# Kernel optimization log

Hardware: AMD Instinct MI355X
Metric: run time of the kernel (lower is better)

## Reference

```python
import jax, jax.numpy as jnp
from jax import lax
import numpy as np

B, IMG, P, CIN, D, DEPTH, H, FF = 32, 512, 16, 4, 256, 4, 8, 2048
N = (IMG // P) ** 2          # 1024 patches
L = N // 2                   # exactly 512 masked patches per batch (static max_len)
DH = D // H
EPS = 1e-5


def layer_norm(x, s, b):
    m = x.mean(-1, keepdims=True)
    v = ((x - m) ** 2).mean(-1, keepdims=True)
    return (x - m) * lax.rsqrt(v + EPS) * s + b


def setup_inputs() -> dict:
    key = jax.random.key(0)
    ks = jax.random.split(key, 16)
    init = lambda k, shp: 0.02 * jax.random.normal(k, shp, jnp.float32)

    image = jax.random.normal(ks[0], (B, 3, IMG, IMG), jnp.float32)
    # patch-granular binary mask: exactly L patches per batch have value 0 (masked)
    scores = jax.random.uniform(ks[1], (B, N))
    idx = jnp.argsort(scores, axis=1)[:, :L]
    pm = jnp.ones((B, N), jnp.float32).at[jnp.arange(B)[:, None], idx].set(0.0)
    mask = jnp.repeat(jnp.repeat(pm.reshape(B, 1, IMG // P, IMG // P), P, 2), P, 3)

    return dict(
        image=image, mask=mask,
        conv_w=init(ks[2], (D, CIN, P, P)), conv_b=jnp.zeros((D,), jnp.float32),
        pos_embed=jax.random.normal(ks[3], (1, N, D), jnp.float32),
        qkv_w=init(ks[4], (DEPTH, D, 3 * D)), qkv_b=jnp.zeros((DEPTH, 3 * D), jnp.float32),
        out_w=init(ks[5], (DEPTH, D, D)), out_b=jnp.zeros((DEPTH, D), jnp.float32),
        ln1_s=jnp.ones((DEPTH, D), jnp.float32), ln1_b=jnp.zeros((DEPTH, D), jnp.float32),
        ff1_w=init(ks[6], (DEPTH, D, FF)), ff1_b=jnp.zeros((DEPTH, FF), jnp.float32),
        ff2_w=init(ks[7], (DEPTH, FF, D)), ff2_b=jnp.zeros((DEPTH, D), jnp.float32),
        ln2_s=jnp.ones((DEPTH, D), jnp.float32), ln2_b=jnp.zeros((DEPTH, D), jnp.float32),
    )


def reference(image, mask, conv_w, conv_b, pos_embed, qkv_w, qkv_b, out_w, out_b,
              ln1_s, ln1_b, ff1_w, ff1_b, ff2_w, ff2_b, ln2_s, ln2_b):
    xin = jnp.concatenate([image, mask], axis=1)                       # [B,4,512,512]
    x = lax.conv_general_dilated(xin, conv_w, (P, P), 'VALID',
                                 dimension_numbers=('NCHW', 'OIHW', 'NCHW'))
    x = x + conv_b[None, :, None, None]                                # [B,D,32,32]
    Bc = x.shape[0]
    x = x.reshape(Bc, D, N).transpose(0, 2, 1)                         # [B,N,D]

    # nearest downsample (factor exactly P): sample at indices i*P
    pmask = mask[:, 0, ::P, ::P].reshape(Bc, N)
    sel = pmask < 0.5                                                  # masked patches
    # stable compaction: indices of masked patches first, in original order
    order = jnp.argsort(jnp.logical_not(sel), axis=1, stable=True)[:, :L]
    tokens = jnp.take_along_axis(x, order[..., None], axis=1)          # [B,L,D]
    pos = pos_embed[0][order]                                          # [B,L,D]
    lengths = sel.sum(axis=1)
    valid = (jnp.arange(L)[None, :] < lengths[:, None])[..., None]
    h = jnp.where(valid, tokens + pos, 0.0)                            # zero padding

    scale = 1.0 / np.sqrt(DH)
    for i in range(DEPTH):  # post-norm torch TransformerEncoderLayer, no dropout
        qkv = h @ qkv_w[i] + qkv_b[i]
        q, k, v = jnp.split(qkv, 3, axis=-1)
        q = q.reshape(Bc, L, H, DH)
        k = k.reshape(Bc, L, H, DH)
        v = v.reshape(Bc, L, H, DH)
        att = jax.nn.softmax(jnp.einsum('bqhd,bkhd->bhqk', q, k) * scale, axis=-1)
        o = jnp.einsum('bhqk,bkhd->bqhd', att, v).reshape(Bc, L, D)
        h = layer_norm(h + o @ out_w[i] + out_b[i], ln1_s[i], ln1_b[i])
        ff = jax.nn.relu(h @ ff1_w[i] + ff1_b[i]) @ ff2_w[i] + ff2_b[i]
        h = layer_norm(h + ff, ln2_s[i], ln2_b[i])
    return h
```

## Files before the change

kernel.cpp:

```cpp
#include <hip/hip_runtime.h>
#include <cstdint>
#include <cstddef>


#define Bq 32
#define Dm 256
#define Lq 512
#define Hh 8
#define FFq 2048
#define Mtok (Bq * Lq)

typedef __attribute__((ext_vector_type(8))) short  short8;
typedef __attribute__((ext_vector_type(4))) float  f32x4;
typedef __attribute__((ext_vector_type(4))) unsigned int u32x4;
typedef __attribute__((ext_vector_type(2))) unsigned int u32x2;

static __device__ __forceinline__ unsigned short f2bf(float f) {
    unsigned int u = __float_as_uint(f);
    unsigned int r = (u + 0x7FFFu + ((u >> 16) & 1u)) >> 16;
    return (unsigned short)r;
}
static __device__ __forceinline__ unsigned int pk2bf(float lo, float hi) {
    return (unsigned int)f2bf(lo) | ((unsigned int)f2bf(hi) << 16);
}

static __device__ __forceinline__ void gload_lds16(const void* g, void* l) {
    __builtin_amdgcn_global_load_lds(
        (const __attribute__((address_space(1))) unsigned int*)g,
        (__attribute__((address_space(3))) unsigned int*)l, 16, 0, 0);
}

static __device__ __forceinline__ int xcd_swz(int id, int grid) {
    return (id & 7) * (grid >> 3) + (id >> 3);
}

__global__ __launch_bounds__(1024) void k_order(const float* __restrict__ mask,
                                                int* __restrict__ order) {
    const int b = blockIdx.x;
    const int n = threadIdx.x;
    const float v = mask[(size_t)b * 262144 + (size_t)(n >> 5) * 8192 + (n & 31) * 16];
    const bool sel = v < 0.5f;
    const unsigned long long ball = __ballot(sel);
    const int wave = n >> 6, lane = n & 63;
    __shared__ int wsum[16];
    __shared__ int wpre[16];
    if (lane == 0) wsum[wave] = __popcll(ball);
    __syncthreads();
    if (n == 0) {
        int s = 0;
        for (int i = 0; i < 16; ++i) { wpre[i] = s; s += wsum[i]; }
    }
    __syncthreads();
    const int rank = wpre[wave] + __popcll(ball & ((1ull << lane) - 1ull));
    if (sel) order[b * Lq + rank] = n;
}

__global__ __launch_bounds__(256) void k_gather(const float* __restrict__ image,
                                                const int* __restrict__ order,
                                                const float* __restrict__ pos,
                                                unsigned short* __restrict__ patchA,
                                                float* __restrict__ posG) {
    __shared__ int pn[16];
    const int tid = threadIdx.x;
    const int tok0 = blockIdx.x * 16;
    if (tid < 16) pn[tid] = order[tok0 + tid];
    __syncthreads();
    const int lane = tid & 63, w4 = tid >> 6;
    const int rr = lane >> 2, col4 = (lane & 3) << 2;
#pragma unroll
    for (int it = 0; it < 12; ++it) {
        const int s = it * 4 + w4;
        const int t = s / 3, cch = s % 3;
        const int n = pn[t];
        const int b = (tok0 + t) >> 9;
        const int pi = n >> 5, pj = n & 31;
        const float4 v = *(const float4*)&image[
            (((size_t)b * 3 + cch) * 512 + pi * 16 + rr) * 512 + pj * 16 + col4];
        unsigned int pk[2] = {pk2bf(v.x, v.y), pk2bf(v.z, v.w)};
        *(uint2*)&patchA[(size_t)(tok0 + t) * 768 + cch * 256 + rr * 16 + col4] =
            *(uint2*)pk;
    }
#pragma unroll
    for (int it = 0; it < 4; ++it) {
        const int t = it * 4 + w4;
        *(float4*)&posG[(size_t)(tok0 + t) * Dm + lane * 4] =
            *(const float4*)&pos[(size_t)pn[t] * Dm + lane * 4];
    }
}

__global__ __launch_bounds__(256) void k_wembed(const float* __restrict__ conv_w,
                                                unsigned short* __restrict__ W16) {
    const int i = blockIdx.x * 256 + threadIdx.x;
    const int d = i / 96, k8 = (i % 96) * 8;
    const float4 a = *(const float4*)&conv_w[(size_t)d * 1024 + k8];
    const float4 b = *(const float4*)&conv_w[(size_t)d * 1024 + k8 + 4];
    unsigned int pk[4] = {pk2bf(a.x, a.y), pk2bf(a.z, a.w),
                          pk2bf(b.x, b.y), pk2bf(b.z, b.w)};
    *(uint4*)&W16[(size_t)d * 768 + k8] = *(uint4*)pk;
}

__global__ __launch_bounds__(256) void k_wprep_all(const float* __restrict__ qkv_w,
                                                   const float* __restrict__ out_w,
                                                   const float* __restrict__ ff1_w,
                                                   const float* __restrict__ ff2_w,
                                                   unsigned short* __restrict__ Wq,
                                                   unsigned short* __restrict__ Wo,
                                                   unsigned short* __restrict__ Wf1,
                                                   unsigned short* __restrict__ Wf2) {
    __shared__ float tile[64][65];
    int idx = blockIdx.x;
    const float* W; unsigned short* WT; int K, N, l, r;
    if (idx < 192)      { l = idx / 48;          r = idx % 48;  K = 256;  N = 768;  W = qkv_w; WT = Wq; }
    else if (idx < 256) { l = (idx - 192) / 16;  r = idx & 15;  K = 256;  N = 256;  W = out_w; WT = Wo; }
    else if (idx < 768) { l = (idx - 256) / 128; r = (idx - 256) % 128; K = 256;  N = 2048; W = ff1_w; WT = Wf1; }
    else                { l = (idx - 768) / 128; r = (idx - 768) % 128; K = 2048; N = 256;  W = ff2_w; WT = Wf2; }
    const int nTiles = N >> 6;
    const int n0 = (r % nTiles) * 64, k0 = (r / nTiles) * 64;
    W  += (size_t)l * K * N;
    WT += (size_t)l * K * N;
    const int t = threadIdx.x;
#pragma unroll
    for (int it = 0; it < 4; ++it) {
        const int rr = (t >> 4) + it * 16, c4 = (t & 15) * 4;
        *(float4*)&tile[rr][c4] = *(const float4*)&W[(size_t)(k0 + rr) * N + n0 + c4];
    }
    __syncthreads();
    const int n = t & 63, kq = t >> 6;
    unsigned short pk[16];
#pragma unroll
    for (int j = 0; j < 16; ++j) pk[j] = f2bf(tile[kq * 16 + j][n]);
    unsigned short* dst = &WT[(size_t)(n0 + n) * K + k0 + kq * 16];
    *(uint4*)dst       = *(uint4*)&pk[0];
    *(uint4*)(dst + 8) = *(uint4*)&pk[8];
}

template <bool RELU, bool RES, bool OUT32, bool OUT16, int NBUF, bool SWZ>
__global__ __launch_bounds__(256) void k_mgemm(const unsigned short* __restrict__ A,
                                               const unsigned short* __restrict__ W,
                                               const float* __restrict__ bias,
                                               const float* __restrict__ R,
                                               float* __restrict__ C32,
                                               unsigned short* __restrict__ C16,
                                               int ntiles, int M, int N, int K) {
    __shared__ unsigned short Al[128 * 64 * NBUF];
    __shared__ unsigned short Bl[128 * 64 * NBUF];
    const int tid = threadIdx.x;
    const int lane = tid & 63, wave = tid >> 6;
    const int wm = wave >> 1, wn = wave & 1;
    int id = blockIdx.x;
    if constexpr (SWZ) id = xcd_swz(id, (int)gridDim.x);
    const int n0 = (id % ntiles) * 128, m0 = (id / ntiles) * 128;
    const int c = lane >> 4, a15 = lane & 15;
    f32x4 acc[4][4] = {};

    const int srow = lane >> 3;
    const int sgran = (lane & 7) ^ srow;
    const int KT = K >> 6;

    auto stage = [&](int buf, int kt) {
        const int k0 = kt << 6;
#pragma unroll
        for (int q = 0; q < 4; ++q) {
            const int rbase = wave * 32 + q * 8;
            gload_lds16(A + (size_t)(m0 + rbase + srow) * K + k0 + sgran * 8,
                        &Al[buf * 8192 + rbase * 64]);
            gload_lds16(W + (size_t)(n0 + rbase + srow) * K + k0 + sgran * 8,
                        &Bl[buf * 8192 + rbase * 64]);
        }
    };
    auto compute = [&](int buf) {
        const int bo = buf * 8192;
#pragma unroll
        for (int kc = 0; kc < 2; ++kc) {
            short8 af[4], bf[4];
#pragma unroll
            for (int fm = 0; fm < 4; ++fm) {
                const int row = wm * 64 + fm * 16 + a15;
                const int slot = (kc * 4 + c) ^ (row & 7);
                af[fm] = *(const short8*)&Al[bo + row * 64 + slot * 8];
            }
#pragma unroll
            for (int fn = 0; fn < 4; ++fn) {
                const int row = wn * 64 + fn * 16 + a15;
                const int slot = (kc * 4 + c) ^ (row & 7);
                bf[fn] = *(const short8*)&Bl[bo + row * 64 + slot * 8];
            }
#pragma unroll
            for (int fm = 0; fm < 4; ++fm)
#pragma unroll
                for (int fn = 0; fn < 4; ++fn)
                    acc[fm][fn] = __builtin_amdgcn_mfma_f32_16x16x32_bf16(
                        af[fm], bf[fn], acc[fm][fn], 0, 0, 0);
        }
    };

    if constexpr (NBUF == 2) {
        stage(0, 0);
        for (int kt = 0; kt < KT; ++kt) {
            const int cur = kt & 1;
            if (kt + 1 < KT) {
                stage(cur ^ 1, kt + 1);
                asm volatile("s_waitcnt vmcnt(8)" ::: "memory");
            } else {
                asm volatile("s_waitcnt vmcnt(0)" ::: "memory");
            }
            __builtin_amdgcn_s_barrier();
            compute(cur);
            __builtin_amdgcn_s_barrier();
        }
    } else {
        for (int kt = 0; kt < KT; ++kt) {
            __syncthreads();
            stage(0, kt);
            __syncthreads();
            compute(0);
        }
    }
#pragma unroll
    for (int fn = 0; fn < 4; ++fn) {
        const int col = n0 + wn * 64 + fn * 16 + a15;
        const float bv = bias[col];
#pragma unroll
        for (int fm = 0; fm < 4; ++fm) {
            const int mrow = m0 + wm * 64 + fm * 16 + c * 4;
#pragma unroll
            for (int r = 0; r < 4; ++r) {
                float v = acc[fm][fn][r] + bv;
                if constexpr (RES) v += R[(size_t)(mrow + r) * N + col];
                if constexpr (RELU) v = fmaxf(v, 0.f);
                if constexpr (OUT32) C32[(size_t)(mrow + r) * N + col] = v;
                if constexpr (OUT16) C16[(size_t)(mrow + r) * N + col] = f2bf(v);
            }
        }
    }
}

template <bool RELU, bool OUT16>
__global__ __launch_bounds__(512) void k_mgemm8(const unsigned short* __restrict__ A,
                                                const unsigned short* __restrict__ W,
                                                const float* __restrict__ bias,
                                                unsigned short* __restrict__ C16,
                                                int ntiles, int N, int K) {
    __shared__ unsigned short Al[256 * 64];
    __shared__ unsigned short Bl[128 * 64];
    const int tid = threadIdx.x;
    const int lane = tid & 63, wave = tid >> 6;
    const int wm = wave >> 1, wn = wave & 1;
    const int id = xcd_swz((int)blockIdx.x, (int)gridDim.x);
    const int n0 = (id % ntiles) * 128, m0 = (id / ntiles) * 256;
    const int c = lane >> 4, a15 = lane & 15;
    f32x4 acc[4][4] = {};

    const int srow = lane >> 3;
    const int sgran = (lane & 7) ^ srow;
    const int KT = K >> 6;

    for (int kt = 0; kt < KT; ++kt) {
        const int k0 = kt << 6;
        __syncthreads();
#pragma unroll
        for (int q = 0; q < 4; ++q) {
            const int rbase = wave * 32 + q * 8;
            gload_lds16(A + (size_t)(m0 + rbase + srow) * K + k0 + sgran * 8,
                        &Al[rbase * 64]);
        }
#pragma unroll
        for (int q = 0; q < 2; ++q) {
            const int rbase = wave * 16 + q * 8;
            gload_lds16(W + (size_t)(n0 + rbase + srow) * K + k0 + sgran * 8,
                        &Bl[rbase * 64]);
        }
        __syncthreads();
#pragma unroll
        for (int kc = 0; kc < 2; ++kc) {
            short8 af[4], bf[4];
#pragma unroll
            for (int fm = 0; fm < 4; ++fm) {
                const int row = wm * 64 + fm * 16 + a15;
                const int slot = (kc * 4 + c) ^ (row & 7);
                af[fm] = *(const short8*)&Al[row * 64 + slot * 8];
            }
#pragma unroll
            for (int fn = 0; fn < 4; ++fn) {
                const int row = wn * 64 + fn * 16 + a15;
                const int slot = (kc * 4 + c) ^ (row & 7);
                bf[fn] = *(const short8*)&Bl[row * 64 + slot * 8];
            }
#pragma unroll
            for (int fm = 0; fm < 4; ++fm)
#pragma unroll
                for (int fn = 0; fn < 4; ++fn)
                    acc[fm][fn] = __builtin_amdgcn_mfma_f32_16x16x32_bf16(
                        af[fm], bf[fn], acc[fm][fn], 0, 0, 0);
        }
    }
#pragma unroll
    for (int fn = 0; fn < 4; ++fn) {
        const int col = n0 + wn * 64 + fn * 16 + a15;
        const float bv = bias[col];
#pragma unroll
        for (int fm = 0; fm < 4; ++fm) {
            const int mrow = m0 + wm * 64 + fm * 16 + c * 4;
#pragma unroll
            for (int r = 0; r < 4; ++r) {
                float v = acc[fm][fn][r] + bv;
                if constexpr (RELU) v = fmaxf(v, 0.f);
                if constexpr (OUT16) C16[(size_t)(mrow + r) * N + col] = f2bf(v);
            }
        }
    }
}

__global__ __launch_bounds__(256) void k_gemm_ln(const unsigned short* __restrict__ A,
                                                 const unsigned short* __restrict__ W,
                                                 const float* __restrict__ bias,
                                                 const float* __restrict__ R,
                                                 const float* __restrict__ lns,
                                                 const float* __restrict__ lnb,
                                                 float* __restrict__ Y32,
                                                 unsigned short* __restrict__ Y16,
                                                 int K) {
    __shared__ unsigned short Al[32 * 64 * 2];
    __shared__ unsigned short Bl[256 * 64 * 2];
    __shared__ float redS[4][32];
    __shared__ float redQ[4][32];
    const int tid = threadIdx.x;
    const int lane = tid & 63, wave = tid >> 6;
    const int m0 = xcd_swz((int)blockIdx.x, (int)gridDim.x) * 32;
    const int c = lane >> 4, a15 = lane & 15;
    f32x4 acc[2][4] = {};

    const int srow = lane >> 3;
    const int sgran = (lane & 7) ^ srow;
    const int KT = K >> 6;

    auto stage = [&](int buf, int kt) {
        const int k0 = kt << 6;
        gload_lds16(A + (size_t)(m0 + wave * 8 + srow) * K + k0 + sgran * 8,
                    &Al[buf * 2048 + (wave * 8) * 64]);
#pragma unroll
        for (int q = 0; q < 8; ++q) {
            const int rbase = wave * 64 + q * 8;
            gload_lds16(W + (size_t)(rbase + srow) * K + k0 + sgran * 8,
                        &Bl[buf * 16384 + rbase * 64]);
        }
    };
    auto compute = [&](int buf) {
        const int ao = buf * 2048, bo = buf * 16384;
#pragma unroll
        for (int kc = 0; kc < 2; ++kc) {
            short8 af[2], bf[4];
#pragma unroll
            for (int fm = 0; fm < 2; ++fm) {
                const int row = fm * 16 + a15;
                const int slot = (kc * 4 + c) ^ (row & 7);
                af[fm] = *(const short8*)&Al[ao + row * 64 + slot * 8];
            }
#pragma unroll
            for (int fn = 0; fn < 4; ++fn) {
                const int row = wave * 64 + fn * 16 + a15;
                const int slot = (kc * 4 + c) ^ (row & 7);
                bf[fn] = *(const short8*)&Bl[bo + row * 64 + slot * 8];
            }
#pragma unroll
            for (int fm = 0; fm < 2; ++fm)
#pragma unroll
                for (int fn = 0; fn < 4; ++fn)
                    acc[fm][fn] = __builtin_amdgcn_mfma_f32_16x16x32_bf16(
                        af[fm], bf[fn], acc[fm][fn], 0, 0, 0);
        }
    };

    stage(0, 0);
    for (int kt = 0; kt < KT; ++kt) {
        const int cur = kt & 1;
        if (kt + 1 < KT) {
            stage(cur ^ 1, kt + 1);
            asm volatile("s_waitcnt vmcnt(9)" ::: "memory");
        } else {
            asm volatile("s_waitcnt vmcnt(0)" ::: "memory");
        }
        __builtin_amdgcn_s_barrier();
        compute(cur);
        __builtin_amdgcn_s_barrier();
    }

    float bv[4], sg[4], bg[4];
#pragma unroll
    for (int fn = 0; fn < 4; ++fn) {
        const int col = wave * 64 + fn * 16 + a15;
        bv[fn] = bias[col]; sg[fn] = lns[col]; bg[fn] = lnb[col];
    }
#pragma unroll
    for (int fm = 0; fm < 2; ++fm) {
        const int mrow = m0 + fm * 16 + c * 4;
#pragma unroll
        for (int r = 0; r < 4; ++r) {
            float ps = 0.f, pq = 0.f;
#pragma unroll
            for (int fn = 0; fn < 4; ++fn) {
                const int col = wave * 64 + fn * 16 + a15;
                float v = acc[fm][fn][r] + bv[fn] + R[(size_t)(mrow + r) * Dm + col];
                acc[fm][fn][r] = v;
                ps += v; pq += v * v;
            }
#pragma unroll
            for (int off = 1; off < 16; off <<= 1) {
                ps += __shfl_xor(ps, off);
                pq += __shfl_xor(pq, off);
            }
            if (a15 == 0) {
                redS[wave][fm * 16 + c * 4 + r] = ps;
                redQ[wave][fm * 16 + c * 4 + r] = pq;
            }
        }
    }
    __syncthreads();
#pragma unroll
    for (int fm = 0; fm < 2; ++fm) {
        const int lrow = fm * 16 + c * 4;
        const int mrow = m0 + lrow;
#pragma unroll
        for (int r = 0; r < 4; ++r) {
            const float totS = redS[0][lrow + r] + redS[1][lrow + r] +
                               redS[2][lrow + r] + redS[3][lrow + r];
            const float totQ = redQ[0][lrow + r] + redQ[1][lrow + r] +
                               redQ[2][lrow + r] + redQ[3][lrow + r];
            const float mean = totS * (1.f / 256.f);
            const float var = totQ * (1.f / 256.f) - mean * mean;
            const float inv = rsqrtf(var + 1e-5f);
#pragma unroll
            for (int fn = 0; fn < 4; ++fn) {
                const int col = wave * 64 + fn * 16 + a15;
                const float y = (acc[fm][fn][r] - mean) * inv * sg[fn] + bg[fn];
                Y32[(size_t)(mrow + r) * Dm + col] = y;
                Y16[(size_t)(mrow + r) * Dm + col] = f2bf(y);
            }
        }
    }
}

__global__ __launch_bounds__(512) void k_attn(const unsigned short* __restrict__ QKV,
                                              unsigned short* __restrict__ O) {
    __shared__ unsigned short Kl[512 * 32];
    __shared__ unsigned short Vt[32 * 512];
    const int bh = xcd_swz((int)blockIdx.x, (int)gridDim.x);
    const int b = bh >> 3, h = bh & 7;
    const int tid = threadIdx.x, lane = tid & 63, wave = tid >> 6;
    const int c = lane >> 4, a15 = lane & 15;
    const size_t qkvbase = (size_t)b * Lq * 768 + h * 32;

    {
        const int srow = lane >> 2;
        const int sg = (lane & 3) ^ ((srow >> 1) & 3);
#pragma unroll
        for (int q = 0; q < 4; ++q) {
            const int rbase = wave * 64 + q * 16;
            gload_lds16(QKV + qkvbase + (size_t)(rbase + srow) * 768 + 256 + sg * 8,
                        &Kl[rbase * 32]);
        }
    }
    {
        const int kg = tid & 127, dg = tid >> 7;
        u32x4 v[4];
#pragma unroll
        for (int kk = 0; kk < 4; ++kk)
            v[kk] = *(const u32x4*)&QKV[qkvbase + (size_t)(kg * 4 + kk) * 768 + 512 + dg * 8];
#pragma unroll
        for (int dd = 0; dd < 8; ++dd) {
            const int d = dg * 8 + dd;
            unsigned short e[4];
#pragma unroll
            for (int kk = 0; kk < 4; ++kk) {
                const unsigned int word = v[kk][dd >> 1];
                e[kk] = (dd & 1) ? (unsigned short)(word >> 16) : (unsigned short)(word & 0xffff);
            }
            unsigned int pk[2];
            pk[0] = (unsigned int)e[0] | ((unsigned int)e[1] << 16);
            pk[1] = (unsigned int)e[2] | ((unsigned int)e[3] << 16);
            *(uint2*)&Vt[d * 512 + ((kg ^ (d & 7)) << 2)] = *(uint2*)pk;
        }
    }
    const int q0w = wave * 64;
    short8 qf[4];
#pragma unroll
    for (int fn = 0; fn < 4; ++fn)
        qf[fn] = *(const short8*)&QKV[qkvbase + (size_t)(q0w + fn * 16 + a15) * 768 + c * 8];
    __syncthreads();

    const float scale = 0.17677669529663687f;
    f32x4 oacc[2][4] = {};
    float mstat[4], lstat[4];
#pragma unroll
    for (int fn = 0; fn < 4; ++fn) { mstat[fn] = -1e30f; lstat[fn] = 0.f; }
    const f32x4 zero4 = {0.f, 0.f, 0.f, 0.f};

    for (int t = 0; t < 16; ++t) {
        const int kv0 = t * 32;
        short8 kf[2];
#pragma unroll
        for (int fm = 0; fm < 2; ++fm) {
            const int row = kv0 + fm * 16 + a15;
            const int slot = c ^ ((row >> 1) & 3);
            kf[fm] = *(const short8*)&Kl[row * 32 + slot * 8];
        }
        short8 vf[2];
#pragma unroll
        for (int fmd = 0; fmd < 2; ++fmd) {
            const int d = fmd * 16 + a15;
            const int g0 = (t * 8 + c) ^ (d & 7);
            const int g1 = (t * 8 + 4 + c) ^ (d & 7);
            const u32x2 r0 = *(const u32x2*)&Vt[d * 512 + g0 * 4];
            const u32x2 r1 = *(const u32x2*)&Vt[d * 512 + g1 * 4];
            const u32x4 cmb = {r0[0], r0[1], r1[0], r1[1]};
            vf[fmd] = __builtin_bit_cast(short8, cmb);
        }
        f32x4 s[2][4];
#pragma unroll
        for (int fm = 0; fm < 2; ++fm)
#pragma unroll
            for (int fn = 0; fn < 4; ++fn)
                s[fm][fn] = __builtin_amdgcn_mfma_f32_16x16x32_bf16(kf[fm], qf[fn], zero4, 0, 0, 0);
#pragma unroll
        for (int fn = 0; fn < 4; ++fn) {
            float p[8];
            float tmax = -1e30f;
#pragma unroll
            for (int fm = 0; fm < 2; ++fm)
#pragma unroll
                for (int r = 0; r < 4; ++r) {
                    const float x = s[fm][fn][r] * scale;
                    p[fm * 4 + r] = x;
                    tmax = fmaxf(tmax, x);
                }
            tmax = fmaxf(tmax, __shfl_xor(tmax, 16));
            tmax = fmaxf(tmax, __shfl_xor(tmax, 32));
            const float mnew = fmaxf(mstat[fn], tmax);
            const float alpha = __expf(mstat[fn] - mnew);
            mstat[fn] = mnew;
            float tsum = 0.f;
            short8 pf;
#pragma unroll
            for (int j = 0; j < 8; ++j) {
                const float e = __expf(p[j] - mnew);
                tsum += e;
                pf[j] = (short)f2bf(e);
            }
            tsum += __shfl_xor(tsum, 16);
            tsum += __shfl_xor(tsum, 32);
            lstat[fn] = lstat[fn] * alpha + tsum;
#pragma unroll
            for (int fmd = 0; fmd < 2; ++fmd) {
                oacc[fmd][fn] *= alpha;
                oacc[fmd][fn] = __builtin_amdgcn_mfma_f32_16x16x32_bf16(
                    vf[fmd], pf, oacc[fmd][fn], 0, 0, 0);
            }
        }
    }
#pragma unroll
    for (int fn = 0; fn < 4; ++fn) {
        const float invl = 1.f / lstat[fn];
        const size_t qrow = (size_t)(b * Lq + q0w + fn * 16 + a15);
#pragma unroll
        for (int fmd = 0; fmd < 2; ++fmd)
#pragma unroll
            for (int r = 0; r < 4; ++r)
                O[qrow * Dm + h * 32 + fmd * 16 + c * 4 + r] = f2bf(oacc[fmd][fn][r] * invl);
    }
}

extern "C" void kernel_launch(void* const* d_in, const int* in_sizes, int n_in,
                              void* d_out, int out_size, void* d_ws, size_t ws_size,
                              hipStream_t stream) {
    const float* image  = (const float*)d_in[0];
    const float* mask   = (const float*)d_in[1];
    const float* conv_w = (const float*)d_in[2];
    const float* conv_b = (const float*)d_in[3];
    const float* pos    = (const float*)d_in[4];
    const float* qkv_w  = (const float*)d_in[5];
    const float* qkv_b  = (const float*)d_in[6];
    const float* out_w  = (const float*)d_in[7];
    const float* out_b  = (const float*)d_in[8];
    const float* ln1_s  = (const float*)d_in[9];
    const float* ln1_b  = (const float*)d_in[10];
    const float* ff1_w  = (const float*)d_in[11];
    const float* ff1_b  = (const float*)d_in[12];
    const float* ff2_w  = (const float*)d_in[13];
    const float* ff2_b  = (const float*)d_in[14];
    const float* ln2_s  = (const float*)d_in[15];
    const float* ln2_b  = (const float*)d_in[16];
    float* out = (float*)d_out;

    char* w = (char*)d_ws;
    int* order            = (int*)w;            w += 64 * 1024;
    float* H32            = (float*)w;          w += (size_t)Mtok * Dm * 4;
    unsigned short* H16   = (unsigned short*)w; w += (size_t)Mtok * Dm * 2;
    unsigned short* QKV16 = (unsigned short*)w; w += (size_t)Mtok * 768 * 2;
    unsigned short* O16   = (unsigned short*)w; w += (size_t)Mtok * Dm * 2;
    unsigned short* F16   = (unsigned short*)w; w += (size_t)Mtok * FFq * 2;
    unsigned short* Wq    = (unsigned short*)w; w += (size_t)4 * 768 * 256 * 2;
    unsigned short* Wo    = (unsigned short*)w; w += (size_t)4 * 256 * 256 * 2;
    unsigned short* Wf1   = (unsigned short*)w; w += (size_t)4 * 2048 * 256 * 2;
    unsigned short* Wf2   = (unsigned short*)w; w += (size_t)4 * 256 * 2048 * 2;
    unsigned short* We    = (unsigned short*)w; w += (size_t)256 * 768 * 2;
    unsigned short* patchA = F16;
    float* posG            = (float*)(F16 + (size_t)Mtok * 768);

    k_order<<<Bq, 1024, 0, stream>>>(mask, order);
    k_gather<<<Mtok / 16, 256, 0, stream>>>(image, order, pos, patchA, posG);
    k_wembed<<<96, 256, 0, stream>>>(conv_w, We);
    k_wprep_all<<<1280, 256, 0, stream>>>(qkv_w, out_w, ff1_w, ff2_w, Wq, Wo, Wf1, Wf2);

    k_mgemm<false, true, true, true, 2, true><<<256, 256, 0, stream>>>(
        patchA, We, conv_b, posG, H32, H16, 2, Mtok, 256, 768);

    for (int i = 0; i < 4; ++i) {
        k_mgemm8<false, true><<<384, 512, 0, stream>>>(
            H16, Wq + (size_t)i * 768 * 256, qkv_b + (size_t)i * 768,
            QKV16, 6, 768, 256);
        k_attn<<<Bq * Hh, 512, 0, stream>>>(QKV16, O16);
        k_gemm_ln<<<Mtok / 32, 256, 0, stream>>>(
            O16, Wo + (size_t)i * 256 * 256, out_b + (size_t)i * 256, H32,
            ln1_s + i * Dm, ln1_b + i * Dm, H32, H16, 256);
        k_mgemm8<true, true><<<1024, 512, 0, stream>>>(
            H16, Wf1 + (size_t)i * 2048 * 256, ff1_b + (size_t)i * FFq,
            F16, 16, 2048, 256);
        float* dst32 = (i == 3) ? out : H32;
        k_gemm_ln<<<Mtok / 32, 256, 0, stream>>>(
            F16, Wf2 + (size_t)i * 256 * 2048, ff2_b + (size_t)i * 256, H32,
            ln2_s + i * Dm, ln2_b + i * Dm, dst32, H16, 2048);
    }
    (void)in_sizes; (void)n_in; (void)out_size; (void)ws_size;
}
```

Measured before the change: 552.6 us.

## Widen fused GEMM+LayerNorm tile to 64 rows with 8 waves

The fused GEMM+residual+LayerNorm kernel now processes 64 rows per block with 512 threads in a 2x4 wave grid, instead of 32 rows with 4 waves. Each staged weight tile is shared by twice as many rows, which halves total weight traffic from global memory into LDS. The grid shrinks from 512 to 256 blocks, roughly one per CU, and LDS use per block rises. This may reduce occupancy and latency hiding.

```diff
diff --git a/kernel.cpp b/kernel.cpp
--- a/kernel.cpp
+++ b/kernel.cpp
@@ -311,22 +311,23 @@
     }
 }
 
-__global__ __launch_bounds__(256) void k_gemm_ln(const unsigned short* __restrict__ A,
-                                                 const unsigned short* __restrict__ W,
-                                                 const float* __restrict__ bias,
-                                                 const float* __restrict__ R,
-                                                 const float* __restrict__ lns,
-                                                 const float* __restrict__ lnb,
-                                                 float* __restrict__ Y32,
-                                                 unsigned short* __restrict__ Y16,
-                                                 int K) {
-    __shared__ unsigned short Al[32 * 64 * 2];
+__global__ __launch_bounds__(512) void k_gemm_ln8(const unsigned short* __restrict__ A,
+                                                  const unsigned short* __restrict__ W,
+                                                  const float* __restrict__ bias,
+                                                  const float* __restrict__ R,
+                                                  const float* __restrict__ lns,
+                                                  const float* __restrict__ lnb,
+                                                  float* __restrict__ Y32,
+                                                  unsigned short* __restrict__ Y16,
+                                                  int K) {
+    __shared__ unsigned short Al[64 * 64 * 2];
     __shared__ unsigned short Bl[256 * 64 * 2];
-    __shared__ float redS[4][32];
-    __shared__ float redQ[4][32];
+    __shared__ float redS[8][32];
+    __shared__ float redQ[8][32];
     const int tid = threadIdx.x;
     const int lane = tid & 63, wave = tid >> 6;
-    const int m0 = xcd_swz((int)blockIdx.x, (int)gridDim.x) * 32;
+    const int wm = wave >> 2, wn = wave & 3;
+    const int m0 = xcd_swz((int)blockIdx.x, (int)gridDim.x) * 64;
     const int c = lane >> 4, a15 = lane & 15;
     f32x4 acc[2][4] = {};
 
@@ -337,28 +338,28 @@
     auto stage = [&](int buf, int kt) {
         const int k0 = kt << 6;
         gload_lds16(A + (size_t)(m0 + wave * 8 + srow) * K + k0 + sgran * 8,
-                    &Al[buf * 2048 + (wave * 8) * 64]);
-#pragma unroll
-        for (int q = 0; q < 8; ++q) {
-            const int rbase = wave * 64 + q * 8;
+                    &Al[buf * 4096 + (wave * 8) * 64]);
+#pragma unroll
+        for (int q = 0; q < 4; ++q) {
+            const int rbase = wave * 32 + q * 8;
             gload_lds16(W + (size_t)(rbase + srow) * K + k0 + sgran * 8,
                         &Bl[buf * 16384 + rbase * 64]);
         }
     };
     auto compute = [&](int buf) {
-        const int ao = buf * 2048, bo = buf * 16384;
+        const int ao = buf * 4096, bo = buf * 16384;
 #pragma unroll
         for (int kc = 0; kc < 2; ++kc) {
             short8 af[2], bf[4];
 #pragma unroll
             for (int fm = 0; fm < 2; ++fm) {
-                const int row = fm * 16 + a15;
+                const int row = wm * 32 + fm * 16 + a15;
                 const int slot = (kc * 4 + c) ^ (row & 7);
                 af[fm] = *(const short8*)&Al[ao + row * 64 + slot * 8];
             }
 #pragma unroll
             for (int fn = 0; fn < 4; ++fn) {
-                const int row = wave * 64 + fn * 16 + a15;
+                const int row = wn * 64 + fn * 16 + a15;
                 const int slot = (kc * 4 + c) ^ (row & 7);
                 bf[fn] = *(const short8*)&Bl[bo + row * 64 + slot * 8];
             }
@@ -376,7 +377,7 @@
         const int cur = kt & 1;
         if (kt + 1 < KT) {
             stage(cur ^ 1, kt + 1);
-            asm volatile("s_waitcnt vmcnt(9)" ::: "memory");
+            asm volatile("s_waitcnt vmcnt(5)" ::: "memory");
         } else {
             asm volatile("s_waitcnt vmcnt(0)" ::: "memory");
         }
@@ -388,18 +389,18 @@
     float bv[4], sg[4], bg[4];
 #pragma unroll
     for (int fn = 0; fn < 4; ++fn) {
-        const int col = wave * 64 + fn * 16 + a15;
+        const int col = wn * 64 + fn * 16 + a15;
         bv[fn] = bias[col]; sg[fn] = lns[col]; bg[fn] = lnb[col];
     }
 #pragma unroll
     for (int fm = 0; fm < 2; ++fm) {
-        const int mrow = m0 + fm * 16 + c * 4;
+        const int mrow = m0 + wm * 32 + fm * 16 + c * 4;
 #pragma unroll
         for (int r = 0; r < 4; ++r) {
             float ps = 0.f, pq = 0.f;
 #pragma unroll
             for (int fn = 0; fn < 4; ++fn) {
-                const int col = wave * 64 + fn * 16 + a15;
+                const int col = wn * 64 + fn * 16 + a15;
                 float v = acc[fm][fn][r] + bv[fn] + R[(size_t)(mrow + r) * Dm + col];
                 acc[fm][fn][r] = v;
                 ps += v; pq += v * v;
@@ -419,19 +420,20 @@
 #pragma unroll
     for (int fm = 0; fm < 2; ++fm) {
         const int lrow = fm * 16 + c * 4;
-        const int mrow = m0 + lrow;
+        const int mrow = m0 + wm * 32 + lrow;
 #pragma unroll
         for (int r = 0; r < 4; ++r) {
-            const float totS = redS[0][lrow + r] + redS[1][lrow + r] +
-                               redS[2][lrow + r] + redS[3][lrow + r];
-            const float totQ = redQ[0][lrow + r] + redQ[1][lrow + r] +
-                               redQ[2][lrow + r] + redQ[3][lrow + r];
+            const int g = wm * 4;
+            const float totS = redS[g + 0][lrow + r] + redS[g + 1][lrow + r] +
+                               redS[g + 2][lrow + r] + redS[g + 3][lrow + r];
+            const float totQ = redQ[g + 0][lrow + r] + redQ[g + 1][lrow + r] +
+                               redQ[g + 2][lrow + r] + redQ[g + 3][lrow + r];
             const float mean = totS * (1.f / 256.f);
             const float var = totQ * (1.f / 256.f) - mean * mean;
             const float inv = rsqrtf(var + 1e-5f);
 #pragma unroll
             for (int fn = 0; fn < 4; ++fn) {
-                const int col = wave * 64 + fn * 16 + a15;
+                const int col = wn * 64 + fn * 16 + a15;
                 const float y = (acc[fm][fn][r] - mean) * inv * sg[fn] + bg[fn];
                 Y32[(size_t)(mrow + r) * Dm + col] = y;
                 Y16[(size_t)(mrow + r) * Dm + col] = f2bf(y);
@@ -619,14 +621,14 @@
             H16, Wq + (size_t)i * 768 * 256, qkv_b + (size_t)i * 768,
             QKV16, 6, 768, 256);
         k_attn<<<Bq * Hh, 512, 0, stream>>>(QKV16, O16);
-        k_gemm_ln<<<Mtok / 32, 256, 0, stream>>>(
+        k_gemm_ln8<<<Mtok / 64, 512, 0, stream>>>(
             O16, Wo + (size_t)i * 256 * 256, out_b + (size_t)i * 256, H32,
             ln1_s + i * Dm, ln1_b + i * Dm, H32, H16, 256);
         k_mgemm8<true, true><<<1024, 512, 0, stream>>>(
             H16, Wf1 + (size_t)i * 2048 * 256, ff1_b + (size_t)i * FFq,
             F16, 16, 2048, 256);
         float* dst32 = (i == 3) ? out : H32;
-        k_gemm_ln<<<Mtok / 32, 256, 0, stream>>>(
+        k_gemm_ln8<<<Mtok / 64, 512, 0, stream>>>(
             F16, Wf2 + (size_t)i * 256 * 2048, ff2_b + (size_t)i * 256, H32,
             ln2_s + i * Dm, ln2_b + i * Dm, dst32, H16, 2048);
     }
```

New measurement: 563.9 us. 2.0% more time.
